# Kernel tuning notes

Hardware: AMD Instinct MI355X
Metric: run time of the kernel (lower is better)

## Reference

```python
import jax, jax.numpy as jnp
import numpy as np

B, N, DIM, T, H, DH = 4, 2048, 512, 16, 8, 64
EPS = 1e-5


def setup_inputs() -> dict:
    key = jax.random.key(0)
    ks = jax.random.split(key, 7)
    x = jax.random.normal(ks[0], (B, N, DIM), dtype=jnp.float32)
    # time-distance matrix, e.g. months between scans, in [0, 24)
    R = jax.random.uniform(ks[1], (B, T, T), dtype=jnp.float32) * 24.0
    gamma = jnp.ones((DIM,), dtype=jnp.float32)
    beta = jnp.zeros((DIM,), dtype=jnp.float32)
    W_qkv = jax.random.normal(ks[2], (DIM, 3 * H * DH), dtype=jnp.float32) * 0.02
    W_out = jax.random.normal(ks[3], (H * DH, DIM), dtype=jnp.float32) * 0.02
    a = jax.random.uniform(ks[4], (H,), dtype=jnp.float32)          # torch.rand(heads)
    c = 12.0 * jax.random.uniform(ks[5], (H,), dtype=jnp.float32)   # 12 * torch.rand(heads)
    return {"x": x, "R": R, "gamma": gamma, "beta": beta,
            "W_qkv": W_qkv, "W_out": W_out, "a": a, "c": c}


def reference(x, R, gamma, beta, W_qkv, W_out, a, c):
    b, n, dim = x.shape
    t = R.shape[-1]
    num_patches = n // t
    scale = DH ** -0.5

    # LayerNorm
    mu = jnp.mean(x, axis=-1, keepdims=True)
    var = jnp.mean(jnp.square(x - mu), axis=-1, keepdims=True)
    xn = (x - mu) * jax.lax.rsqrt(var + EPS) * gamma + beta

    # QKV projection -> [b, h, n, d]
    qkv = xn @ W_qkv  # [b, n, 3*h*d]
    q, k, v = jnp.split(qkv, 3, axis=-1)
    def to_heads(z):
        return z.reshape(b, n, H, DH).transpose(0, 2, 1, 3)
    q, k, v = to_heads(q), to_heads(k), to_heads(v)

    # attention scores with ReLU then learned sigmoid time-decay mask
    dots = jnp.einsum('bhnd,bhmd->bhnm', q, k) * scale
    dots = jax.nn.relu(dots)

    # flipped-sigmoid decay: 1 / (1 + exp(|a|*R - |c|)), per head  -> [b, h, t, t]
    decay = 1.0 / (1.0 + jnp.exp(jnp.abs(a)[None, :, None, None] * R[:, None, :, :]
                                 - jnp.abs(c)[None, :, None, None]))
    # expand timepoint mask to token resolution (repeat_interleave on both axes)
    decay = jnp.repeat(jnp.repeat(decay, num_patches, axis=2), num_patches, axis=3)

    attn = jax.nn.softmax(dots * decay, axis=-1)
    out = jnp.einsum('bhnm,bhmd->bhnd', attn, v)
    out = out.transpose(0, 2, 1, 3).reshape(b, n, H * DH)
    return out @ W_out  # dropout is identity at eval
```

## Files before the change

kernel.cpp:

```cpp
#include <hip/hip_runtime.h>
#include <math.h>

#define B_   4
#define N_   2048
#define DIM_ 512
#define T_   16
#define H_   8
#define DH_  64

typedef unsigned short ushort_t;
typedef __attribute__((ext_vector_type(8))) short bf16x8;
typedef __attribute__((ext_vector_type(16))) float f32x16;

__device__ inline ushort_t bf16_rn(float x) {
  unsigned u = __builtin_bit_cast(unsigned, x);
  u += 0x7FFFu + ((u >> 16) & 1u);
  return (ushort_t)(u >> 16);
}
__device__ inline float bf16f(ushort_t h) {
  return __builtin_bit_cast(float, (unsigned)h << 16);
}
__device__ inline unsigned pack2(ushort_t a, ushort_t b) {
  return (unsigned)a | ((unsigned)b << 16);
}
__device__ inline void split2(float x, ushort_t &h, ushort_t &l) {
  h = bf16_rn(x);
  l = bf16_rn(x - bf16f(h));
}
__device__ inline unsigned cvt_pk_bf16(float lo, float hi) {
  unsigned r;
  asm("v_cvt_pk_bf16_f32 %0, %1, %2" : "=v"(r) : "v"(lo), "v"(hi));
  return r;
}
__device__ inline void permlane32_swap(unsigned &x, unsigned &y) {
  asm volatile("v_permlane32_swap_b32 %0, %1" : "+v"(x), "+v"(y));
}

__global__ __launch_bounds__(256) void prep_kernel(
    const float* __restrict__ x, const float* __restrict__ gamma,
    const float* __restrict__ beta, const float* __restrict__ Wqkv,
    const float* __restrict__ Wout,
    ushort_t* __restrict__ xnh, ushort_t* __restrict__ xnl,
    ushort_t* __restrict__ wqh, ushort_t* __restrict__ wql,
    ushort_t* __restrict__ woh, ushort_t* __restrict__ wol) {
  __shared__ float Ts[64][68];
  int bidx = blockIdx.x;
  int tid = threadIdx.x;
  if (bidx < 256) {
    const float* src; ushort_t* dh; ushort_t* dl; int Nn, n0, k0;
    if (bidx < 192) {
      src = Wqkv; dh = wqh; dl = wql; Nn = 1536;
      n0 = (bidx % 24) * 64; k0 = (bidx / 24) * 64;
    } else {
      int l = bidx - 192;
      src = Wout; dh = woh; dl = wol; Nn = 512;
      n0 = (l % 8) * 64; k0 = (l / 8) * 64;
    }
#pragma unroll
    for (int it = 0; it < 4; ++it) {
      int idx = tid + it * 256;
      int r = idx >> 4, c4 = (idx & 15) * 4;
      *(float4*)&Ts[r][c4] = *(const float4*)&src[(size_t)(k0 + r) * Nn + n0 + c4];
    }
    __syncthreads();
#pragma unroll
    for (int it = 0; it < 2; ++it) {
      int idx = tid + it * 256;
      int n = idx >> 3, kc = (idx & 7) * 8;
      ushort_t hs[8], ls[8];
#pragma unroll
      for (int j = 0; j < 8; ++j) split2(Ts[kc + j][n], hs[j], ls[j]);
      uint4 uh, ul;
      uh.x = pack2(hs[0], hs[1]); uh.y = pack2(hs[2], hs[3]);
      uh.z = pack2(hs[4], hs[5]); uh.w = pack2(hs[6], hs[7]);
      ul.x = pack2(ls[0], ls[1]); ul.y = pack2(ls[2], ls[3]);
      ul.z = pack2(ls[4], ls[5]); ul.w = pack2(ls[6], ls[7]);
      size_t o = (size_t)(n0 + n) * 512 + k0 + kc;
      *(uint4*)&dh[o] = uh;
      *(uint4*)&dl[o] = ul;
    }
  } else {
    int row  = (bidx - 256) * 4 + (tid >> 6);
    int lane = tid & 63;
    const float4* xr = (const float4*)(x + (size_t)row * DIM_);
    float4 v0 = xr[lane * 2 + 0];
    float4 v1 = xr[lane * 2 + 1];
    float s  = v0.x + v0.y + v0.z + v0.w + v1.x + v1.y + v1.z + v1.w;
    float ss = v0.x*v0.x + v0.y*v0.y + v0.z*v0.z + v0.w*v0.w
             + v1.x*v1.x + v1.y*v1.y + v1.z*v1.z + v1.w*v1.w;
#pragma unroll
    for (int off = 32; off > 0; off >>= 1) {
      s  += __shfl_xor(s, off);
      ss += __shfl_xor(ss, off);
    }
    float mu  = s * (1.0f / DIM_);
    float var = ss * (1.0f / DIM_) - mu * mu;
    float rstd = rsqrtf(var + 1e-5f);
    float4 g0 = *(const float4*)&gamma[lane * 8];
    float4 g1 = *(const float4*)&gamma[lane * 8 + 4];
    float4 b0 = *(const float4*)&beta[lane * 8];
    float4 b1 = *(const float4*)&beta[lane * 8 + 4];
    float xv[8] = {v0.x, v0.y, v0.z, v0.w, v1.x, v1.y, v1.z, v1.w};
    float gv[8] = {g0.x, g0.y, g0.z, g0.w, g1.x, g1.y, g1.z, g1.w};
    float bv[8] = {b0.x, b0.y, b0.z, b0.w, b1.x, b1.y, b1.z, b1.w};
    ushort_t hs[8], ls[8];
#pragma unroll
    for (int j = 0; j < 8; ++j) {
      float xn = (xv[j] - mu) * rstd * gv[j] + bv[j];
      split2(xn, hs[j], ls[j]);
    }
    uint4 uh, ul;
    uh.x = pack2(hs[0], hs[1]); uh.y = pack2(hs[2], hs[3]);
    uh.z = pack2(hs[4], hs[5]); uh.w = pack2(hs[6], hs[7]);
    ul.x = pack2(ls[0], ls[1]); ul.y = pack2(ls[2], ls[3]);
    ul.z = pack2(ls[4], ls[5]); ul.w = pack2(ls[6], ls[7]);
    size_t o = (size_t)row * DIM_ + lane * 8;
    *(uint4*)&xnh[o] = uh;
    *(uint4*)&xnl[o] = ul;
  }
}

__global__ __launch_bounds__(256) void qkv_gemm_mfma(
    const ushort_t* __restrict__ xnh, const ushort_t* __restrict__ xnl,
    const ushort_t* __restrict__ wth, const ushort_t* __restrict__ wtl,
    ushort_t* __restrict__ qh, ushort_t* __restrict__ ql,
    ushort_t* __restrict__ kho, ushort_t* __restrict__ klo,
    ushort_t* __restrict__ vt) {
  __shared__ ushort_t Ah[128 * 40], Al[128 * 40], Bh[128 * 40], Bl[128 * 40];
  int tid = threadIdx.x;
  int w = tid >> 6, lane = tid & 63, l31 = lane & 31, g = lane >> 5;
  int wm = w >> 1, wn = w & 1;
  int idx = blockIdx.x;
  int xcd = idx & 7, local = idx >> 3;
  int n0 = (local % 12) * 128;
  int m0 = ((local / 12) * 8 + xcd) * 128;

  f32x16 acc[2][2];
#pragma unroll
  for (int i = 0; i < 2; ++i)
#pragma unroll
    for (int j = 0; j < 2; ++j)
#pragma unroll
      for (int e = 0; e < 16; ++e) acc[i][j][e] = 0.0f;

  int fm[2], fc[2];
#pragma unroll
  for (int it = 0; it < 2; ++it) {
    int f = tid + it * 256;
    fm[it] = f >> 2;
    fc[it] = (f & 3) * 8;
  }

#pragma unroll 1
  for (int kt = 0; kt < 16; ++kt) {
    __syncthreads();
#pragma unroll
    for (int it = 0; it < 2; ++it) {
      size_t ao = (size_t)(m0 + fm[it]) * 512 + kt * 32 + fc[it];
      size_t bo = (size_t)(n0 + fm[it]) * 512 + kt * 32 + fc[it];
      uint4 tah = *(const uint4*)&xnh[ao];
      uint4 tal = *(const uint4*)&xnl[ao];
      uint4 tbh = *(const uint4*)&wth[bo];
      uint4 tbl = *(const uint4*)&wtl[bo];
      int o = fm[it] * 40 + fc[it];
      *(uint4*)&Ah[o] = tah;
      *(uint4*)&Al[o] = tal;
      *(uint4*)&Bh[o] = tbh;
      *(uint4*)&Bl[o] = tbl;
    }
    __syncthreads();
#pragma unroll
    for (int kc = 0; kc < 2; ++kc) {
      int off = kc * 16 + 8 * g;
      bf16x8 afh[2], afl[2], bfh[2], bfl[2];
#pragma unroll
      for (int rb = 0; rb < 2; ++rb) {
        int r = (wm * 64 + rb * 32 + l31) * 40 + off;
        afh[rb] = *(const bf16x8*)&Ah[r];
        afl[rb] = *(const bf16x8*)&Al[r];
      }
#pragma unroll
      for (int cb = 0; cb < 2; ++cb) {
        int r = (wn * 64 + cb * 32 + l31) * 40 + off;
        bfh[cb] = *(const bf16x8*)&Bh[r];
        bfl[cb] = *(const bf16x8*)&Bl[r];
      }
#pragma unroll
      for (int rb = 0; rb < 2; ++rb)
#pragma unroll
        for (int cb = 0; cb < 2; ++cb) {
          acc[rb][cb] = __builtin_amdgcn_mfma_f32_32x32x16_bf16(afh[rb], bfh[cb], acc[rb][cb], 0, 0, 0);
          acc[rb][cb] = __builtin_amdgcn_mfma_f32_32x32x16_bf16(afh[rb], bfl[cb], acc[rb][cb], 0, 0, 0);
          acc[rb][cb] = __builtin_amdgcn_mfma_f32_32x32x16_bf16(afl[rb], bfh[cb], acc[rb][cb], 0, 0, 0);
        }
    }
  }

  int part = n0 >> 9;
#pragma unroll
  for (int rb = 0; rb < 2; ++rb) {
    int m_base = m0 + wm * 64 + rb * 32;
#pragma unroll
    for (int cb = 0; cb < 2; ++cb) {
      int n_g = n0 + wn * 64 + cb * 32 + l31;
      int rem = n_g & 511, hh = rem >> 6, d = rem & 63;
      if (part == 2) {
#pragma unroll
        for (int grp = 0; grp < 4; ++grp) {
          int m_g = m_base + grp * 8 + 4 * g;
          int bb = m_g >> 11, tok = m_g & 2047;
          uint2 pk;
          pk.x = pack2(bf16_rn(acc[rb][cb][grp * 4 + 0]), bf16_rn(acc[rb][cb][grp * 4 + 1]));
          pk.y = pack2(bf16_rn(acc[rb][cb][grp * 4 + 2]), bf16_rn(acc[rb][cb][grp * 4 + 3]));
          *(uint2*)&vt[((size_t)(bb * 8 + hh) * 64 + d) * 2048 + tok] = pk;
        }
      } else {
        float sc = (part == 0) ? 0.125f : 1.0f;
        ushort_t* dsth = (part == 0) ? qh : kho;
        ushort_t* dstl = (part == 0) ? ql : klo;
#pragma unroll
        for (int reg = 0; reg < 16; ++reg) {
          int row = (reg & 3) + 8 * (reg >> 2) + 4 * g;
          int m_g = m_base + row;
          int bb = m_g >> 11, tok = m_g & 2047;
          ushort_t hi, lo;
          split2(acc[rb][cb][reg] * sc, hi, lo);
          size_t addr = ((size_t)(bb * 8 + hh) * 2048 + tok) * 64 + d;
          dsth[addr] = hi;
          dstl[addr] = lo;
        }
      }
    }
  }
}

__global__ __launch_bounds__(256) void attn_mfma(
    const ushort_t* __restrict__ qh, const ushort_t* __restrict__ ql,
    const ushort_t* __restrict__ kho, const ushort_t* __restrict__ klo,
    const ushort_t* __restrict__ vt, const float* __restrict__ R,
    const float* __restrict__ a, const float* __restrict__ c,
    ushort_t* __restrict__ aoh, ushort_t* __restrict__ aol) {
  __shared__ ushort_t KhS[64 * 72], KlS[64 * 72], VtS[64 * 72];
  __shared__ float rsS[128];

  int tid = threadIdx.x;
  int w = tid >> 6, lane = tid & 63, l31 = lane & 31, g = lane >> 5;
  int bh = blockIdx.x;
  int qt = blockIdx.y;
  int b = bh >> 3, h = bh & 7;
  float aab = fabsf(a[h]);
  float cab = fabsf(c[h]);

  int qrow = qt * 128 + w * 32 + l31;
  size_t qoff = ((size_t)bh * 2048 + qrow) * 64;
  bf16x8 qfh[4], qfl[4];
#pragma unroll
  for (int d0i = 0; d0i < 4; ++d0i) {
    qfh[d0i] = *(const bf16x8*)&qh[qoff + d0i * 16 + 8 * g];
    qfl[d0i] = *(const bf16x8*)&ql[qoff + d0i * 16 + 8 * g];
  }

  const ushort_t* kbase = kho + (size_t)bh * 2048 * 64;
  const ushort_t* lbase = klo + (size_t)bh * 2048 * 64;
  const ushort_t* vbase = vt + (size_t)bh * 64 * 2048;

  f32x16 oacc[2];
#pragma unroll
  for (int t = 0; t < 2; ++t)
#pragma unroll
    for (int i = 0; i < 16; ++i) oacc[t][i] = 0.0f;
  float rs = 0.0f;

  int frow[2], fcc[2];
#pragma unroll
  for (int it = 0; it < 2; ++it) {
    int idx = tid + it * 256;
    frow[it] = idx >> 3;
    fcc[it] = (idx & 7) * 8;
  }

#pragma unroll 1
  for (int kt = 0; kt < 32; ++kt) {
    __syncthreads();
#pragma unroll
    for (int it = 0; it < 2; ++it) {
      uint4 tk = *(const uint4*)&kbase[(size_t)(kt * 64 + frow[it]) * 64 + fcc[it]];
      uint4 tl = *(const uint4*)&lbase[(size_t)(kt * 64 + frow[it]) * 64 + fcc[it]];
      uint4 tv = *(const uint4*)&vbase[(size_t)frow[it] * 2048 + kt * 64 + fcc[it]];
      int o = frow[it] * 72 + fcc[it];
      *(uint4*)&KhS[o] = tk;
      *(uint4*)&KlS[o] = tl;
      *(uint4*)&VtS[o] = tv;
    }
    __syncthreads();

    float Rv = R[b * (T_ * T_) + qt * T_ + (kt >> 1)];
    float decl2 = 1.4426950408889634f / (1.0f + __expf(aab * Rv - cab));

    bf16x8 pa[4];
#pragma unroll
    for (int khalf = 0; khalf < 2; ++khalf) {
      f32x16 sacc;
#pragma unroll
      for (int i = 0; i < 16; ++i) sacc[i] = 0.0f;
      int krow = (khalf * 32 + l31) * 72;
#pragma unroll
      for (int d0i = 0; d0i < 4; ++d0i) {
        int off = krow + d0i * 16 + 8 * g;
        bf16x8 kfh = *(const bf16x8*)&KhS[off];
        bf16x8 kfl = *(const bf16x8*)&KlS[off];
        sacc = __builtin_amdgcn_mfma_f32_32x32x16_bf16(kfh, qfh[d0i], sacc, 0, 0, 0);
        sacc = __builtin_amdgcn_mfma_f32_32x32x16_bf16(kfl, qfh[d0i], sacc, 0, 0, 0);
        sacc = __builtin_amdgcn_mfma_f32_32x32x16_bf16(kfh, qfl[d0i], sacc, 0, 0, 0);
      }
#pragma unroll
      for (int reg = 0; reg < 16; ++reg) {
        float pv = exp2f(fmaxf(sacc[reg], 0.0f) * decl2);
        rs += pv;
        sacc[reg] = pv;
      }
#pragma unroll
      for (int hf = 0; hf < 2; ++hf) {
        unsigned d0 = cvt_pk_bf16(sacc[hf * 8 + 0], sacc[hf * 8 + 1]);
        unsigned d1 = cvt_pk_bf16(sacc[hf * 8 + 2], sacc[hf * 8 + 3]);
        unsigned d2 = cvt_pk_bf16(sacc[hf * 8 + 4], sacc[hf * 8 + 5]);
        unsigned d3 = cvt_pk_bf16(sacc[hf * 8 + 6], sacc[hf * 8 + 7]);
        permlane32_swap(d0, d2);
        permlane32_swap(d1, d3);
        uint4 u; u.x = d0; u.y = d1; u.z = d2; u.w = d3;
        pa[khalf * 2 + hf] = __builtin_bit_cast(bf16x8, u);
      }
    }

#pragma unroll
    for (int dt = 0; dt < 2; ++dt) {
      int vrow = (dt * 32 + l31) * 72;
#pragma unroll
      for (int kc = 0; kc < 4; ++kc) {
        bf16x8 vf = *(const bf16x8*)&VtS[vrow + kc * 16 + 8 * g];
        oacc[dt] = __builtin_amdgcn_mfma_f32_32x32x16_bf16(pa[kc], vf, oacc[dt], 0, 0, 0);
      }
    }
  }

  rs += __shfl_xor(rs, 32);
  rsS[w * 32 + l31] = rs;

#pragma unroll
  for (int reg = 0; reg < 16; ++reg) {
    int row = (reg & 3) + 8 * (reg >> 2) + 4 * g;
    float invs = 1.0f / rsS[w * 32 + row];
    int tok = qt * 128 + w * 32 + row;
#pragma unroll
    for (int dt = 0; dt < 2; ++dt) {
      int d = dt * 32 + l31;
      ushort_t hi, lo;
      split2(oacc[dt][reg] * invs, hi, lo);
      size_t addr = ((size_t)b * 2048 + tok) * 512 + h * 64 + d;
      aoh[addr] = hi;
      aol[addr] = lo;
    }
  }
}

__global__ __launch_bounds__(256) void out_gemm_mfma(
    const ushort_t* __restrict__ ah, const ushort_t* __restrict__ al,
    const ushort_t* __restrict__ wth, const ushort_t* __restrict__ wtl,
    float* __restrict__ out) {
  __shared__ ushort_t Ah[128 * 40], Al[128 * 40], Bh[128 * 40], Bl[128 * 40];
  int tid = threadIdx.x;
  int w = tid >> 6, lane = tid & 63, l31 = lane & 31, g = lane >> 5;
  int wm = w >> 1, wn = w & 1;
  int idx = blockIdx.x;
  int xcd = idx & 7, local = idx >> 3;
  int n0 = (local & 3) * 128;
  int m0 = ((local >> 2) * 8 + xcd) * 128;

  f32x16 acc[2][2];
#pragma unroll
  for (int i = 0; i < 2; ++i)
#pragma unroll
    for (int j = 0; j < 2; ++j)
#pragma unroll
      for (int e = 0; e < 16; ++e) acc[i][j][e] = 0.0f;

  int fm[2], fc[2];
#pragma unroll
  for (int it = 0; it < 2; ++it) {
    int f = tid + it * 256;
    fm[it] = f >> 2;
    fc[it] = (f & 3) * 8;
  }

#pragma unroll 1
  for (int kt = 0; kt < 16; ++kt) {
    __syncthreads();
#pragma unroll
    for (int it = 0; it < 2; ++it) {
      size_t ao = (size_t)(m0 + fm[it]) * 512 + kt * 32 + fc[it];
      size_t bo = (size_t)(n0 + fm[it]) * 512 + kt * 32 + fc[it];
      uint4 tah = *(const uint4*)&ah[ao];
      uint4 tal = *(const uint4*)&al[ao];
      uint4 tbh = *(const uint4*)&wth[bo];
      uint4 tbl = *(const uint4*)&wtl[bo];
      int o = fm[it] * 40 + fc[it];
      *(uint4*)&Ah[o] = tah;
      *(uint4*)&Al[o] = tal;
      *(uint4*)&Bh[o] = tbh;
      *(uint4*)&Bl[o] = tbl;
    }
    __syncthreads();
#pragma unroll
    for (int kc = 0; kc < 2; ++kc) {
      int off = kc * 16 + 8 * g;
      bf16x8 afh[2], afl[2], bfh[2], bfl[2];
#pragma unroll
      for (int rb = 0; rb < 2; ++rb) {
        int r = (wm * 64 + rb * 32 + l31) * 40 + off;
        afh[rb] = *(const bf16x8*)&Ah[r];
        afl[rb] = *(const bf16x8*)&Al[r];
      }
#pragma unroll
      for (int cb = 0; cb < 2; ++cb) {
        int r = (wn * 64 + cb * 32 + l31) * 40 + off;
        bfh[cb] = *(const bf16x8*)&Bh[r];
        bfl[cb] = *(const bf16x8*)&Bl[r];
      }
#pragma unroll
      for (int rb = 0; rb < 2; ++rb)
#pragma unroll
        for (int cb = 0; cb < 2; ++cb) {
          acc[rb][cb] = __builtin_amdgcn_mfma_f32_32x32x16_bf16(afh[rb], bfh[cb], acc[rb][cb], 0, 0, 0);
          acc[rb][cb] = __builtin_amdgcn_mfma_f32_32x32x16_bf16(afh[rb], bfl[cb], acc[rb][cb], 0, 0, 0);
          acc[rb][cb] = __builtin_amdgcn_mfma_f32_32x32x16_bf16(afl[rb], bfh[cb], acc[rb][cb], 0, 0, 0);
        }
    }
  }

#pragma unroll
  for (int rb = 0; rb < 2; ++rb) {
    int m_base = m0 + wm * 64 + rb * 32;
#pragma unroll
    for (int cb = 0; cb < 2; ++cb) {
      int n_g = n0 + wn * 64 + cb * 32 + l31;
#pragma unroll
      for (int reg = 0; reg < 16; ++reg) {
        int row = (reg & 3) + 8 * (reg >> 2) + 4 * g;
        out[(size_t)(m_base + row) * 512 + n_g] = acc[rb][cb][reg];
      }
    }
  }
}

extern "C" void kernel_launch(void* const* d_in, const int* in_sizes, int n_in,
                              void* d_out, int out_size, void* d_ws, size_t ws_size,
                              hipStream_t stream) {
  (void)in_sizes; (void)n_in;
  const float* x     = (const float*)d_in[0];
  const float* R     = (const float*)d_in[1];
  const float* gamma = (const float*)d_in[2];
  const float* beta  = (const float*)d_in[3];
  const float* Wqkv  = (const float*)d_in[4];
  const float* Wout  = (const float*)d_in[5];
  const float* av    = (const float*)d_in[6];
  const float* cv    = (const float*)d_in[7];
  float* out = (float*)d_out;

  const size_t EL  = (size_t)B_ * N_ * DIM_;
  const size_t SZT = EL * sizeof(ushort_t);

  char* p = (char*)d_ws;
  ushort_t* wqh = (ushort_t*)p;                  p += (size_t)1536 * 512 * 2;
  ushort_t* wql = (ushort_t*)p;                  p += (size_t)1536 * 512 * 2;
  ushort_t* woh = (ushort_t*)p;                  p += (size_t)512 * 512 * 2;
  ushort_t* wol = (ushort_t*)p;                  p += (size_t)512 * 512 * 2;
  ushort_t* qhb = (ushort_t*)p;                  p += SZT;
  ushort_t* qlb = (ushort_t*)p;                  p += SZT;
  ushort_t* khb = (ushort_t*)p;                  p += SZT;
  ushort_t* klb = (ushort_t*)p;                  p += SZT;
  ushort_t* vtb = (ushort_t*)p;                  p += SZT;
  size_t base_need = (size_t)(p - (char*)d_ws);
  size_t needA = base_need + 2 * SZT;

  bool planA = (ws_size >= needA);
  ushort_t* xnh = planA ? (ushort_t*)p : (ushort_t*)d_out;
  ushort_t* xnl = xnh + EL;
  float* gemm_dst = planA ? out : (float*)qhb;

  prep_kernel<<<dim3(2304), dim3(256), 0, stream>>>(x, gamma, beta, Wqkv, Wout,
                                                    xnh, xnl, wqh, wql, woh, wol);
  qkv_gemm_mfma<<<dim3(768), dim3(256), 0, stream>>>(xnh, xnl, wqh, wql,
                                                     qhb, qlb, khb, klb, vtb);
  attn_mfma<<<dim3(32, 16), dim3(256), 0, stream>>>(qhb, qlb, khb, klb, vtb,
                                                    R, av, cv, xnh, xnl);
  out_gemm_mfma<<<dim3(256), dim3(256), 0, stream>>>(xnh, xnl, woh, wol, gemm_dst);
  if (!planA) {
    hipMemcpyAsync(out, gemm_dst, (size_t)out_size * sizeof(float),
                   hipMemcpyDeviceToDevice, stream);
  }
}
```

Measured before the change: 240.4 us.

## Register-prefetch next tiles in GEMM and attention loops, add MFMA priority hints

In the QKV GEMM, the attention kernel and the output GEMM, the global loads for the next K tile are now issued into registers right after the current tile is written to shared memory. Their latency then overlaps with the MFMA work on the current tile instead of stalling at the top of each iteration. MFMA blocks are wrapped in s_setprio(1)/s_setprio(0) so waves issuing matrix ops get scheduling priority. The attention row-sum is split across four partial accumulators to shorten the dependency chain. The cost is extra VGPR pressure, which could lower occupancy.

```diff
diff --git a/kernel.cpp b/kernel.cpp
--- a/kernel.cpp
+++ b/kernel.cpp
@@ -151,22 +151,38 @@
     fc[it] = (f & 3) * 8;
   }
 
+  uint4 tah[2], tal[2], tbh[2], tbl[2];
+#pragma unroll
+  for (int it = 0; it < 2; ++it) {
+    size_t ao = (size_t)(m0 + fm[it]) * 512 + fc[it];
+    size_t bo = (size_t)(n0 + fm[it]) * 512 + fc[it];
+    tah[it] = *(const uint4*)&xnh[ao];
+    tal[it] = *(const uint4*)&xnl[ao];
+    tbh[it] = *(const uint4*)&wth[bo];
+    tbl[it] = *(const uint4*)&wtl[bo];
+  }
+
 #pragma unroll 1
   for (int kt = 0; kt < 16; ++kt) {
     __syncthreads();
 #pragma unroll
     for (int it = 0; it < 2; ++it) {
-      size_t ao = (size_t)(m0 + fm[it]) * 512 + kt * 32 + fc[it];
-      size_t bo = (size_t)(n0 + fm[it]) * 512 + kt * 32 + fc[it];
-      uint4 tah = *(const uint4*)&xnh[ao];
-      uint4 tal = *(const uint4*)&xnl[ao];
-      uint4 tbh = *(const uint4*)&wth[bo];
-      uint4 tbl = *(const uint4*)&wtl[bo];
       int o = fm[it] * 40 + fc[it];
-      *(uint4*)&Ah[o] = tah;
-      *(uint4*)&Al[o] = tal;
-      *(uint4*)&Bh[o] = tbh;
-      *(uint4*)&Bl[o] = tbl;
+      *(uint4*)&Ah[o] = tah[it];
+      *(uint4*)&Al[o] = tal[it];
+      *(uint4*)&Bh[o] = tbh[it];
+      *(uint4*)&Bl[o] = tbl[it];
+    }
+    if (kt + 1 < 16) {
+#pragma unroll
+      for (int it = 0; it < 2; ++it) {
+        size_t ao = (size_t)(m0 + fm[it]) * 512 + (kt + 1) * 32 + fc[it];
+        size_t bo = (size_t)(n0 + fm[it]) * 512 + (kt + 1) * 32 + fc[it];
+        tah[it] = *(const uint4*)&xnh[ao];
+        tal[it] = *(const uint4*)&xnl[ao];
+        tbh[it] = *(const uint4*)&wth[bo];
+        tbl[it] = *(const uint4*)&wtl[bo];
+      }
     }
     __syncthreads();
 #pragma unroll
@@ -185,6 +201,7 @@
         bfh[cb] = *(const bf16x8*)&Bh[r];
         bfl[cb] = *(const bf16x8*)&Bl[r];
       }
+      __builtin_amdgcn_s_setprio(1);
 #pragma unroll
       for (int rb = 0; rb < 2; ++rb)
 #pragma unroll
@@ -193,6 +210,7 @@
           acc[rb][cb] = __builtin_amdgcn_mfma_f32_32x32x16_bf16(afh[rb], bfl[cb], acc[rb][cb], 0, 0, 0);
           acc[rb][cb] = __builtin_amdgcn_mfma_f32_32x32x16_bf16(afl[rb], bfh[cb], acc[rb][cb], 0, 0, 0);
         }
+      __builtin_amdgcn_s_setprio(0);
     }
   }
 
@@ -269,7 +287,7 @@
   for (int t = 0; t < 2; ++t)
 #pragma unroll
     for (int i = 0; i < 16; ++i) oacc[t][i] = 0.0f;
-  float rs = 0.0f;
+  float rsp[4] = {0.0f, 0.0f, 0.0f, 0.0f};
 
   int frow[2], fcc[2];
 #pragma unroll
@@ -279,18 +297,31 @@
     fcc[it] = (idx & 7) * 8;
   }
 
+  uint4 pk[2], pl[2], pv[2];
+#pragma unroll
+  for (int it = 0; it < 2; ++it) {
+    pk[it] = *(const uint4*)&kbase[(size_t)frow[it] * 64 + fcc[it]];
+    pl[it] = *(const uint4*)&lbase[(size_t)frow[it] * 64 + fcc[it]];
+    pv[it] = *(const uint4*)&vbase[(size_t)frow[it] * 2048 + fcc[it]];
+  }
+
 #pragma unroll 1
   for (int kt = 0; kt < 32; ++kt) {
     __syncthreads();
 #pragma unroll
     for (int it = 0; it < 2; ++it) {
-      uint4 tk = *(const uint4*)&kbase[(size_t)(kt * 64 + frow[it]) * 64 + fcc[it]];
-      uint4 tl = *(const uint4*)&lbase[(size_t)(kt * 64 + frow[it]) * 64 + fcc[it]];
-      uint4 tv = *(const uint4*)&vbase[(size_t)frow[it] * 2048 + kt * 64 + fcc[it]];
       int o = frow[it] * 72 + fcc[it];
-      *(uint4*)&KhS[o] = tk;
-      *(uint4*)&KlS[o] = tl;
-      *(uint4*)&VtS[o] = tv;
+      *(uint4*)&KhS[o] = pk[it];
+      *(uint4*)&KlS[o] = pl[it];
+      *(uint4*)&VtS[o] = pv[it];
+    }
+    if (kt + 1 < 32) {
+#pragma unroll
+      for (int it = 0; it < 2; ++it) {
+        pk[it] = *(const uint4*)&kbase[(size_t)((kt + 1) * 64 + frow[it]) * 64 + fcc[it]];
+        pl[it] = *(const uint4*)&lbase[(size_t)((kt + 1) * 64 + frow[it]) * 64 + fcc[it]];
+        pv[it] = *(const uint4*)&vbase[(size_t)frow[it] * 2048 + (kt + 1) * 64 + fcc[it]];
+      }
     }
     __syncthreads();
 
@@ -304,6 +335,7 @@
 #pragma unroll
       for (int i = 0; i < 16; ++i) sacc[i] = 0.0f;
       int krow = (khalf * 32 + l31) * 72;
+      __builtin_amdgcn_s_setprio(1);
 #pragma unroll
       for (int d0i = 0; d0i < 4; ++d0i) {
         int off = krow + d0i * 16 + 8 * g;
@@ -313,11 +345,12 @@
         sacc = __builtin_amdgcn_mfma_f32_32x32x16_bf16(kfl, qfh[d0i], sacc, 0, 0, 0);
         sacc = __builtin_amdgcn_mfma_f32_32x32x16_bf16(kfh, qfl[d0i], sacc, 0, 0, 0);
       }
+      __builtin_amdgcn_s_setprio(0);
 #pragma unroll
       for (int reg = 0; reg < 16; ++reg) {
-        float pv = exp2f(fmaxf(sacc[reg], 0.0f) * decl2);
-        rs += pv;
-        sacc[reg] = pv;
+        float pvv = exp2f(fmaxf(sacc[reg], 0.0f) * decl2);
+        rsp[reg & 3] += pvv;
+        sacc[reg] = pvv;
       }
 #pragma unroll
       for (int hf = 0; hf < 2; ++hf) {
@@ -332,6 +365,7 @@
       }
     }
 
+    __builtin_amdgcn_s_setprio(1);
 #pragma unroll
     for (int dt = 0; dt < 2; ++dt) {
       int vrow = (dt * 32 + l31) * 72;
@@ -341,8 +375,10 @@
         oacc[dt] = __builtin_amdgcn_mfma_f32_32x32x16_bf16(pa[kc], vf, oacc[dt], 0, 0, 0);
       }
     }
-  }
-
+    __builtin_amdgcn_s_setprio(0);
+  }
+
+  float rs = (rsp[0] + rsp[1]) + (rsp[2] + rsp[3]);
   rs += __shfl_xor(rs, 32);
   rsS[w * 32 + l31] = rs;
 
@@ -392,22 +428,38 @@
     fc[it] = (f & 3) * 8;
   }
 
+  uint4 tah[2], tal[2], tbh[2], tbl[2];
+#pragma unroll
+  for (int it = 0; it < 2; ++it) {
+    size_t ao = (size_t)(m0 + fm[it]) * 512 + fc[it];
+    size_t bo = (size_t)(n0 + fm[it]) * 512 + fc[it];
+    tah[it] = *(const uint4*)&ah[ao];
+    tal[it] = *(const uint4*)&al[ao];
+    tbh[it] = *(const uint4*)&wth[bo];
+    tbl[it] = *(const uint4*)&wtl[bo];
+  }
+
 #pragma unroll 1
   for (int kt = 0; kt < 16; ++kt) {
     __syncthreads();
 #pragma unroll
     for (int it = 0; it < 2; ++it) {
-      size_t ao = (size_t)(m0 + fm[it]) * 512 + kt * 32 + fc[it];
-      size_t bo = (size_t)(n0 + fm[it]) * 512 + kt * 32 + fc[it];
-      uint4 tah = *(const uint4*)&ah[ao];
-      uint4 tal = *(const uint4*)&al[ao];
-      uint4 tbh = *(const uint4*)&wth[bo];
-      uint4 tbl = *(const uint4*)&wtl[bo];
       int o = fm[it] * 40 + fc[it];
-      *(uint4*)&Ah[o] = tah;
-      *(uint4*)&Al[o] = tal;
-      *(uint4*)&Bh[o] = tbh;
-      *(uint4*)&Bl[o] = tbl;
+      *(uint4*)&Ah[o] = tah[it];
+      *(uint4*)&Al[o] = tal[it];
+      *(uint4*)&Bh[o] = tbh[it];
+      *(uint4*)&Bl[o] = tbl[it];
+    }
+    if (kt + 1 < 16) {
+#pragma unroll
+      for (int it = 0; it < 2; ++it) {
+        size_t ao = (size_t)(m0 + fm[it]) * 512 + (kt + 1) * 32 + fc[it];
+        size_t bo = (size_t)(n0 + fm[it]) * 512 + (kt + 1) * 32 + fc[it];
+        tah[it] = *(const uint4*)&ah[ao];
+        tal[it] = *(const uint4*)&al[ao];
+        tbh[it] = *(const uint4*)&wth[bo];
+        tbl[it] = *(const uint4*)&wtl[bo];
+      }
     }
     __syncthreads();
 #pragma unroll
@@ -426,6 +478,7 @@
         bfh[cb] = *(const bf16x8*)&Bh[r];
         bfl[cb] = *(const bf16x8*)&Bl[r];
       }
+      __builtin_amdgcn_s_setprio(1);
 #pragma unroll
       for (int rb = 0; rb < 2; ++rb)
 #pragma unroll
@@ -434,6 +487,7 @@
           acc[rb][cb] = __builtin_amdgcn_mfma_f32_32x32x16_bf16(afh[rb], bfl[cb], acc[rb][cb], 0, 0, 0);
           acc[rb][cb] = __builtin_amdgcn_mfma_f32_32x32x16_bf16(afl[rb], bfh[cb], acc[rb][cb], 0, 0, 0);
         }
+      __builtin_amdgcn_s_setprio(0);
     }
   }
 
```

Result: slower. 378.9 us (+57.6%).

## Double-buffer K/V tiles with direct global-to-LDS loads and XOR swizzle

Applied to the files above, without the earlier changes.

The attention kernel now stages K-hi, K-lo and V^T tiles with global_load_lds straight into a double-buffered LDS layout. The next tile is prefetched while the current one is computed, replacing the synchronous register round-trip and the padded stride-72 layout with an XOR-swizzled stride-64 layout. The per-timepoint decay values are precomputed once per block into shared memory, and the row-sum accumulation is split across four partial sums. The aims are to hide global load latency and cut per-iteration sync and exp work. In exchange it doubles LDS use and depends on manual vmcnt counting and raw s_barrier ordering being correct.

```diff
diff --git a/kernel.cpp b/kernel.cpp
--- a/kernel.cpp
+++ b/kernel.cpp
@@ -34,6 +34,12 @@
 }
 __device__ inline void permlane32_swap(unsigned &x, unsigned &y) {
   asm volatile("v_permlane32_swap_b32 %0, %1" : "+v"(x), "+v"(y));
+}
+__device__ inline void gload_lds16(const ushort_t* g, ushort_t* l) {
+  __builtin_amdgcn_global_load_lds(
+      (const __attribute__((address_space(1))) unsigned int*)(g),
+      (__attribute__((address_space(3))) unsigned int*)(l),
+      16, 0, 0);
 }
 
 __global__ __launch_bounds__(256) void prep_kernel(
@@ -240,16 +246,15 @@
     const ushort_t* __restrict__ vt, const float* __restrict__ R,
     const float* __restrict__ a, const float* __restrict__ c,
     ushort_t* __restrict__ aoh, ushort_t* __restrict__ aol) {
-  __shared__ ushort_t KhS[64 * 72], KlS[64 * 72], VtS[64 * 72];
+  __shared__ ushort_t KhS[2 * 4096], KlS[2 * 4096], VtS[2 * 4096];
   __shared__ float rsS[128];
+  __shared__ float decl2S[16];
 
   int tid = threadIdx.x;
   int w = tid >> 6, lane = tid & 63, l31 = lane & 31, g = lane >> 5;
   int bh = blockIdx.x;
   int qt = blockIdx.y;
   int b = bh >> 3, h = bh & 7;
-  float aab = fabsf(a[h]);
-  float cab = fabsf(c[h]);
 
   int qrow = qt * 128 + w * 32 + l31;
   size_t qoff = ((size_t)bh * 2048 + qrow) * 64;
@@ -264,38 +269,57 @@
   const ushort_t* lbase = klo + (size_t)bh * 2048 * 64;
   const ushort_t* vbase = vt + (size_t)bh * 64 * 2048;
 
+  if (tid < 16) {
+    float aab = fabsf(a[h]);
+    float cab = fabsf(c[h]);
+    float Rv = R[b * (T_ * T_) + qt * T_ + tid];
+    decl2S[tid] = 1.4426950408889634f / (1.0f + __expf(aab * Rv - cab));
+  }
+
+  int lr = lane >> 3;
+  int sc = ((lane & 7) ^ lr) * 8;
+  int ci0 = w, ci1 = w + 4;
+  int row0 = ci0 * 8 + lr, row1 = ci1 * 8 + lr;
+
   f32x16 oacc[2];
 #pragma unroll
   for (int t = 0; t < 2; ++t)
 #pragma unroll
     for (int i = 0; i < 16; ++i) oacc[t][i] = 0.0f;
-  float rs = 0.0f;
-
-  int frow[2], fcc[2];
-#pragma unroll
-  for (int it = 0; it < 2; ++it) {
-    int idx = tid + it * 256;
-    frow[it] = idx >> 3;
-    fcc[it] = (idx & 7) * 8;
-  }
+  float rsp[4] = {0.0f, 0.0f, 0.0f, 0.0f};
+
+  {
+    gload_lds16(&kbase[(size_t)(0 * 64 + row0) * 64 + sc], &KhS[ci0 * 512]);
+    gload_lds16(&kbase[(size_t)(0 * 64 + row1) * 64 + sc], &KhS[ci1 * 512]);
+    gload_lds16(&lbase[(size_t)(0 * 64 + row0) * 64 + sc], &KlS[ci0 * 512]);
+    gload_lds16(&lbase[(size_t)(0 * 64 + row1) * 64 + sc], &KlS[ci1 * 512]);
+    gload_lds16(&vbase[(size_t)row0 * 2048 + 0 * 64 + sc], &VtS[ci0 * 512]);
+    gload_lds16(&vbase[(size_t)row1 * 2048 + 0 * 64 + sc], &VtS[ci1 * 512]);
+  }
+  __syncthreads();
+
+  int swz = (l31 & 7) * 8;
+  int cur = 0;
 
 #pragma unroll 1
   for (int kt = 0; kt < 32; ++kt) {
-    __syncthreads();
-#pragma unroll
-    for (int it = 0; it < 2; ++it) {
-      uint4 tk = *(const uint4*)&kbase[(size_t)(kt * 64 + frow[it]) * 64 + fcc[it]];
-      uint4 tl = *(const uint4*)&lbase[(size_t)(kt * 64 + frow[it]) * 64 + fcc[it]];
-      uint4 tv = *(const uint4*)&vbase[(size_t)frow[it] * 2048 + kt * 64 + fcc[it]];
-      int o = frow[it] * 72 + fcc[it];
-      *(uint4*)&KhS[o] = tk;
-      *(uint4*)&KlS[o] = tl;
-      *(uint4*)&VtS[o] = tv;
-    }
-    __syncthreads();
-
-    float Rv = R[b * (T_ * T_) + qt * T_ + (kt >> 1)];
-    float decl2 = 1.4426950408889634f / (1.0f + __expf(aab * Rv - cab));
+    if (kt + 1 < 32) {
+      int base = (cur ^ 1) * 4096;
+      int kk = kt + 1;
+      gload_lds16(&kbase[(size_t)(kk * 64 + row0) * 64 + sc], &KhS[base + ci0 * 512]);
+      gload_lds16(&kbase[(size_t)(kk * 64 + row1) * 64 + sc], &KhS[base + ci1 * 512]);
+      gload_lds16(&lbase[(size_t)(kk * 64 + row0) * 64 + sc], &KlS[base + ci0 * 512]);
+      gload_lds16(&lbase[(size_t)(kk * 64 + row1) * 64 + sc], &KlS[base + ci1 * 512]);
+      gload_lds16(&vbase[(size_t)row0 * 2048 + kk * 64 + sc], &VtS[base + ci0 * 512]);
+      gload_lds16(&vbase[(size_t)row1 * 2048 + kk * 64 + sc], &VtS[base + ci1 * 512]);
+      asm volatile("s_waitcnt vmcnt(6)" ::: "memory");
+    } else {
+      asm volatile("s_waitcnt vmcnt(0)" ::: "memory");
+    }
+    __builtin_amdgcn_s_barrier();
+
+    float decl2 = decl2S[kt >> 1];
+    int kb = cur * 4096;
 
     bf16x8 pa[4];
 #pragma unroll
@@ -303,10 +327,10 @@
       f32x16 sacc;
 #pragma unroll
       for (int i = 0; i < 16; ++i) sacc[i] = 0.0f;
-      int krow = (khalf * 32 + l31) * 72;
+      int krow = kb + (khalf * 32 + l31) * 64;
 #pragma unroll
       for (int d0i = 0; d0i < 4; ++d0i) {
-        int off = krow + d0i * 16 + 8 * g;
+        int off = krow + ((d0i * 16 + 8 * g) ^ swz);
         bf16x8 kfh = *(const bf16x8*)&KhS[off];
         bf16x8 kfl = *(const bf16x8*)&KlS[off];
         sacc = __builtin_amdgcn_mfma_f32_32x32x16_bf16(kfh, qfh[d0i], sacc, 0, 0, 0);
@@ -315,9 +339,9 @@
       }
 #pragma unroll
       for (int reg = 0; reg < 16; ++reg) {
-        float pv = exp2f(fmaxf(sacc[reg], 0.0f) * decl2);
-        rs += pv;
-        sacc[reg] = pv;
+        float pvv = exp2f(fmaxf(sacc[reg], 0.0f) * decl2);
+        rsp[reg & 3] += pvv;
+        sacc[reg] = pvv;
       }
 #pragma unroll
       for (int hf = 0; hf < 2; ++hf) {
@@ -334,15 +358,19 @@
 
 #pragma unroll
     for (int dt = 0; dt < 2; ++dt) {
-      int vrow = (dt * 32 + l31) * 72;
+      int vrow = kb + (dt * 32 + l31) * 64;
 #pragma unroll
       for (int kc = 0; kc < 4; ++kc) {
-        bf16x8 vf = *(const bf16x8*)&VtS[vrow + kc * 16 + 8 * g];
+        bf16x8 vf = *(const bf16x8*)&VtS[vrow + ((kc * 16 + 8 * g) ^ swz)];
         oacc[dt] = __builtin_amdgcn_mfma_f32_32x32x16_bf16(pa[kc], vf, oacc[dt], 0, 0, 0);
       }
     }
-  }
-
+
+    __builtin_amdgcn_s_barrier();
+    cur ^= 1;
+  }
+
+  float rs = (rsp[0] + rsp[1]) + (rsp[2] + rsp[3]);
   rs += __shfl_xor(rs, 32);
   rsS[w * 32 + l31] = rs;
 
```

Result: slower. 249.9 us (+3.9%).
